# Kernel optimization log

Measured on AMD Instinct MI355X. Metric: run time of the kernel, lower is better.

## Reference

```python
import jax, jax.numpy as jnp
import numpy as np

N, E, B = 8000, 24000, 256
ATOM, BOND, H, HEADS, L = 133, 14, 256, 8, 5
NEG, EPS = 0.2, 1e-5


def _ln(x, g, b):
    m = x.mean(-1, keepdims=True)
    v = ((x - m) ** 2).mean(-1, keepdims=True)
    return (x - m) * jax.lax.rsqrt(v + EPS) * g + b


def setup_inputs() -> dict:
    key = jax.random.key(0)
    ks = jax.random.split(key, 12)
    s = lambda k, shp, fan: (jax.random.normal(k, shp, jnp.float32) / np.float32(np.sqrt(fan)))
    inp = {
        "x": jax.random.normal(ks[0], (N, ATOM), jnp.float32),
        "edge_attr": jax.random.normal(ks[1], (E, BOND), jnp.float32),
        "emb_W": s(ks[2], (ATOM, H), ATOM), "emb_b": jnp.zeros((H,), jnp.float32),
        "emb_g": jnp.ones((H,), jnp.float32), "emb_beta": jnp.zeros((H,), jnp.float32),
        "Wl": s(ks[3], (L, H, HEADS * H), H), "Wr": s(ks[4], (L, H, HEADS * H), H),
        "We": s(ks[5], (L, BOND, HEADS * H), BOND),
        "att": s(ks[6], (L, HEADS, H), H),
        "bias": jnp.zeros((L, H), jnp.float32),
        "ln_g": jnp.ones((L, H), jnp.float32), "ln_b": jnp.zeros((L, H), jnp.float32),
        "g1W": s(ks[7], (H, H // 2), H), "g1b": jnp.zeros((H // 2,), jnp.float32),
        "g2W": s(ks[8], (H // 2, 1), H // 2), "g2b": jnp.zeros((1,), jnp.float32),
        "edge_index": jax.random.randint(ks[9], (2, E), 0, N, dtype=jnp.int32),
        "batch_vec": jnp.sort(jax.random.randint(ks[10], (N,), 0, B, dtype=jnp.int32)),
    }
    return inp


def reference(x, edge_attr, emb_W, emb_b, emb_g, emb_beta, Wl, Wr, We, att, bias,
              ln_g, ln_b, g1W, g1b, g2W, g2b, edge_index, batch_vec):
    src, dst = edge_index[0], edge_index[1]
    # GATv2Conv add_self_loops=True, fill_value='mean': self-loop edge_attr at node i
    # is the mean of edge features of edges incoming to i (zeros if none).
    deg = jax.ops.segment_sum(jnp.ones((E,), x.dtype), dst, num_segments=N)
    loop_attr = jax.ops.segment_sum(edge_attr, dst, num_segments=N) / jnp.maximum(deg, 1.0)[:, None]
    ar = jnp.arange(N)
    src_a = jnp.concatenate([src, ar])
    dst_a = jnp.concatenate([dst, ar])
    ea = jnp.concatenate([edge_attr, loop_attr], axis=0)  # [E+N, BOND]
    # atom embedding: Linear -> LayerNorm -> ReLU (dropout = identity at eval)
    h = jax.nn.relu(_ln(x @ emb_W + emb_b, emb_g, emb_beta))  # [N, H]
    for l in range(L):
        xl = (h @ Wl[l]).reshape(N, HEADS, H)  # source transform
        xr = (h @ Wr[l]).reshape(N, HEADS, H)  # destination transform
        ee = (ea @ We[l]).reshape(-1, HEADS, H)
        f = jax.nn.leaky_relu(xl[src_a] + xr[dst_a] + ee, NEG)  # [EA, HEADS, H]
        score = jnp.einsum('ehd,hd->eh', f, att[l])  # [EA, HEADS]
        # scatter-softmax over edges sharing a destination (self-loops => no empty segment)
        m = jax.ops.segment_max(score, dst_a, num_segments=N)
        ex = jnp.exp(score - m[dst_a])
        alpha = ex / jax.ops.segment_sum(ex, dst_a, num_segments=N)[dst_a]
        msg = xl[src_a] * alpha[..., None]
        out = jax.ops.segment_sum(msg, dst_a, num_segments=N).mean(axis=1) + bias[l]  # concat=False: head mean
        h = _ln(out + h, ln_g[l], ln_b[l])  # residual + LayerNorm
    # GlobalAttention readout: gate_nn -> scatter-softmax per graph -> weighted sum
    gate = jax.nn.relu(h @ g1W + g1b) @ g2W + g2b  # [N, 1]
    gm = jax.ops.segment_max(gate, batch_vec, num_segments=B)
    ge = jnp.exp(gate - gm[batch_vec])
    w = ge / jnp.maximum(jax.ops.segment_sum(ge, batch_vec, num_segments=B)[batch_vec], 1e-16)
    return jax.ops.segment_sum(w * h, batch_vec, num_segments=B)  # [B, H]
```

## Files before the change

kernel.cpp:

```cpp
#include <hip/hip_runtime.h>
#include <math.h>

#define N_NODES 8000
#define N_EDGES 24000
#define NB      256
#define ATOM    133
#define BOND    14
#define HDIM    256
#define HEADS   8
#define NLAYERS 5
#define NEG     0.2f
#define LN_EPS  1e-5f
#define HH      (HEADS * HDIM)
#define MPAD    8064

typedef __attribute__((ext_vector_type(8))) short short8;
typedef __attribute__((ext_vector_type(4))) float floatx4;
typedef unsigned short ushort_t;

__device__ __forceinline__ ushort_t f2bf(float f) {
  unsigned u = __float_as_uint(f);
  unsigned r = (u + 0x7fff + ((u >> 16) & 1)) >> 16;
  return (ushort_t)r;
}
__device__ __forceinline__ float bf2f(ushort_t h) {
  return __uint_as_float(((unsigned)h) << 16);
}
__device__ __forceinline__ float4 ldbf4(const ushort_t* p) {
  ushort4 u = *(const ushort4*)p;
  return make_float4(bf2f(u.x), bf2f(u.y), bf2f(u.z), bf2f(u.w));
}

__device__ __forceinline__ void load_lds16(const void* g, void* l) {
  __builtin_amdgcn_global_load_lds((const __attribute__((address_space(1))) unsigned int*)g,
                                   (__attribute__((address_space(3))) unsigned int*)l,
                                   16, 0, 0);
}

__device__ __forceinline__ float block_reduce_sum(float v, float* red) {
  int t = threadIdx.x;
  red[t] = v; __syncthreads();
  for (int s = blockDim.x >> 1; s > 0; s >>= 1) {
    if (t < s) red[t] += red[t + s];
    __syncthreads();
  }
  float r = red[0]; __syncthreads();
  return r;
}
__device__ __forceinline__ float block_reduce_max(float v, float* red) {
  int t = threadIdx.x;
  red[t] = v; __syncthreads();
  for (int s = blockDim.x >> 1; s > 0; s >>= 1) {
    if (t < s) red[t] = fmaxf(red[t], red[t + s]);
    __syncthreads();
  }
  float r = red[0]; __syncthreads();
  return r;
}

__global__ void k_deg(const int* __restrict__ dst, int* __restrict__ deg) {
  int e = blockIdx.x * blockDim.x + threadIdx.x;
  if (e < N_EDGES) atomicAdd(&deg[dst[e]], 1);
}

__global__ void k_scan(const int* __restrict__ cnt, int* __restrict__ offs, int n) {
  __shared__ int wsum[8];
  __shared__ int carry_s;
  int t = threadIdx.x, w = t >> 6, lane = t & 63;
  if (t == 0) carry_s = 0;
  __syncthreads();
  for (int base = 0; base < n; base += 256) {
    int i = base + t;
    int v = (i < n) ? cnt[i] : 0;
    int x = v;
#pragma unroll
    for (int off = 1; off < 64; off <<= 1) {
      int u = __shfl_up(x, off);
      if (lane >= off) x += u;
    }
    if (lane == 63) wsum[w] = x;
    __syncthreads();
    int wpre = 0;
    for (int q = 0; q < w; q++) wpre += wsum[q];
    int carry = carry_s;
    if (i < n) offs[i] = carry + wpre + x - v;
    __syncthreads();
    if (t == 255) carry_s = carry + wpre + x;
    __syncthreads();
  }
  if (t == 0) offs[n] = carry_s;
}

__global__ void k_fill(const int* __restrict__ dst, const int* __restrict__ row_start,
                       int* __restrict__ cursor, int* __restrict__ csr_eid) {
  int e = blockIdx.x * blockDim.x + threadIdx.x;
  if (e < N_EDGES) {
    int d = dst[e];
    int pos = atomicAdd(&cursor[d], 1);
    csr_eid[row_start[d] + pos] = e;
  }
}

__global__ void k_loop_attr(const float* __restrict__ edge_attr, const int* __restrict__ row_start,
                            const int* __restrict__ csr_eid, float* __restrict__ loop_attr) {
  int t = blockIdx.x * blockDim.x + threadIdx.x;
  if (t >= N_NODES * BOND) return;
  int i = t / BOND, k = t % BOND;
  int beg = row_start[i], end = row_start[i + 1];
  float s = 0.f;
  for (int p = beg; p < end; p++) s += edge_attr[(size_t)csr_eid[p] * BOND + k];
  int degv = end - beg;
  loop_attr[(size_t)i * BOND + k] = s / fmaxf((float)degv, 1.f);
}

__global__ __launch_bounds__(256) void k_build_bt(const float* __restrict__ Wl,
                                                  const float* __restrict__ Wr,
                                                  ushort_t* __restrict__ Bt) {
  int l = blockIdx.x >> 12;
  int n = blockIdx.x & 4095;
  int k = threadIdx.x;
  const float* Wsrc = (n < HH) ? Wl : Wr;
  int nn = (n < HH) ? n : n - HH;
  float w = Wsrc[(size_t)l * HDIM * HH + (size_t)k * HH + nn];
  Bt[((size_t)l * 4096 + n) * 256 + k] = f2bf(w);
}

__global__ __launch_bounds__(256) void k_embed(const float* __restrict__ x, const float* __restrict__ W,
                                               const float* __restrict__ b, const float* __restrict__ g,
                                               const float* __restrict__ beta, float* __restrict__ h,
                                               ushort_t* __restrict__ Abuf) {
  __shared__ float xs[ATOM];
  __shared__ float red[256];
  int i = blockIdx.x, j = threadIdx.x;
  if (j < ATOM) xs[j] = x[(size_t)i * ATOM + j];
  __syncthreads();
  float acc = b[j];
  for (int k = 0; k < ATOM; k++) acc += xs[k] * W[(size_t)k * HDIM + j];
  float mean = block_reduce_sum(acc, red) * (1.f / HDIM);
  float diff = acc - mean;
  float var = block_reduce_sum(diff * diff, red) * (1.f / HDIM);
  float vn = diff * rsqrtf(var + LN_EPS) * g[j] + beta[j];
  float r = fmaxf(vn, 0.f);
  h[(size_t)i * HDIM + j] = r;
  Abuf[(size_t)i * 256 + j] = f2bf(r);
}

__global__ __launch_bounds__(256) void k_gemm_mfma(const ushort_t* __restrict__ A,
                                                   const ushort_t* __restrict__ Bt,
                                                   ushort_t* __restrict__ C) {
  __shared__ char smem[34816];
  ushort_t* As = (ushort_t*)smem;
  ushort_t* Bs = (ushort_t*)(smem + 16384);
  ushort_t* Cs = (ushort_t*)smem;
  const int tid = threadIdx.x;
  const int wave = tid >> 6, lane = tid & 63;
  const int bm = blockIdx.y * 128, bn = blockIdx.x * 128;
  const int wm = (wave >> 1) * 64, wn = (wave & 1) * 64;

  const ushort_t* agA[4];
  const ushort_t* agB[4];
  ushort_t* alA[4];
  ushort_t* alB[4];
#pragma unroll
  for (int j = 0; j < 4; j++) {
    int c = j * 256 + tid;
    int row = c >> 3, col = (c & 7) * 8;
    agA[j] = A  + (size_t)(bm + row) * 256 + col;
    agB[j] = Bt + (size_t)(bn + row) * 256 + col;
    alA[j] = As + c * 8;
    alB[j] = Bs + c * 8;
  }

  floatx4 acc[4][4] = {};
  const int mrow = lane & 15;
  const int kq = (lane >> 4) * 8;

  for (int k0 = 0; k0 < 256; k0 += 64) {
#pragma unroll
    for (int j = 0; j < 4; j++) load_lds16(agA[j] + k0, alA[j]);
#pragma unroll
    for (int j = 0; j < 4; j++) load_lds16(agB[j] + k0, alB[j]);
    __syncthreads();
#pragma unroll
    for (int half = 0; half < 2; half++) {
      const int kk = half * 32 + kq;
      short8 af[4], bfr[4];
#pragma unroll
      for (int mi = 0; mi < 4; mi++)
        af[mi] = *(const short8*)&As[(wm + mi * 16 + mrow) * 64 + kk];
#pragma unroll
      for (int ni = 0; ni < 4; ni++)
        bfr[ni] = *(const short8*)&Bs[(wn + ni * 16 + mrow) * 64 + kk];
#pragma unroll
      for (int mi = 0; mi < 4; mi++)
#pragma unroll
        for (int ni = 0; ni < 4; ni++)
          acc[mi][ni] = __builtin_amdgcn_mfma_f32_16x16x32_bf16(af[mi], bfr[ni], acc[mi][ni], 0, 0, 0);
    }
    __syncthreads();
  }
  const int lr = (lane >> 4) * 4, lc = lane & 15;
#pragma unroll
  for (int mi = 0; mi < 4; mi++)
#pragma unroll
    for (int ni = 0; ni < 4; ni++)
#pragma unroll
      for (int r = 0; r < 4; r++)
        Cs[(wm + mi * 16 + lr + r) * 136 + wn + ni * 16 + lc] = f2bf(acc[mi][ni][r]);
  __syncthreads();
#pragma unroll
  for (int it = 0; it < 8; it++) {
    int idx = it * 256 + tid;
    int row = idx >> 4, chunk = idx & 15;
    int grow = bm + row;
    if (grow < N_NODES) {
      short8 v = *(const short8*)&Cs[row * 136 + chunk * 8];
      *(short8*)&C[(size_t)grow * 4096 + bn + chunk * 8] = v;
    }
  }
}

__device__ __forceinline__ float edge_score(float x0, float x1, float x2, float x3,
                                            float r0, float r1, float r2, float r3,
                                            const float eav[BOND], const float wreg[BOND][4],
                                            float a0, float a1, float a2, float a3) {
  float e0 = 0.f, e1 = 0.f, e2 = 0.f, e3 = 0.f;
#pragma unroll
  for (int k = 0; k < BOND; k++) {
    e0 += eav[k] * wreg[k][0]; e1 += eav[k] * wreg[k][1];
    e2 += eav[k] * wreg[k][2]; e3 += eav[k] * wreg[k][3];
  }
  float f0 = x0 + r0 + e0; f0 = f0 > 0.f ? f0 : NEG * f0;
  float f1 = x1 + r1 + e1; f1 = f1 > 0.f ? f1 : NEG * f1;
  float f2 = x2 + r2 + e2; f2 = f2 > 0.f ? f2 : NEG * f2;
  float f3 = x3 + r3 + e3; f3 = f3 > 0.f ? f3 : NEG * f3;
  float sp = f0 * a0 + f1 * a1 + f2 * a2 + f3 * a3;
#pragma unroll
  for (int off = 32; off > 0; off >>= 1) sp += __shfl_xor(sp, off);
  return sp;
}

__device__ __forceinline__ void ld_eav(const float* p, float eav[BOND]) {
#pragma unroll
  for (int k = 0; k < 7; k++) {
    float2 t = *(const float2*)(p + 2 * k);
    eav[2 * k] = t.x; eav[2 * k + 1] = t.y;
  }
}

__global__ __launch_bounds__(512) void k_attn(const ushort_t* __restrict__ xlr,
    const float* __restrict__ edge_attr, const float* __restrict__ loop_attr,
    const float* __restrict__ We, const float* __restrict__ att,
    const int* __restrict__ row_start, const int* __restrict__ csr_eid,
    const int* __restrict__ src, const float* __restrict__ bias,
    const float* __restrict__ lng, const float* __restrict__ lnb,
    float* __restrict__ h, ushort_t* __restrict__ Abuf) {
  __shared__ ushort_t sacc[2][HEADS][264];
  const int tid = threadIdx.x, hh = tid >> 6, lane = tid & 63;
  float wreg[BOND][4];
#pragma unroll
  for (int k = 0; k < BOND; k++) {
    float4 t = *(const float4*)&We[(size_t)k * HH + hh * HDIM + lane * 4];
    wreg[k][0] = t.x; wreg[k][1] = t.y; wreg[k][2] = t.z; wreg[k][3] = t.w;
  }
  float4 at4 = *(const float4*)&att[hh * HDIM + lane * 4];
  const int node0 = blockIdx.x * 2;

#pragma unroll
  for (int ni = 0; ni < 2; ni++) {
    int i = node0 + ni;
    int beg = row_start[i], end = row_start[i + 1];
    float4 xr4 = ldbf4(&xlr[(size_t)i * 4096 + 2048 + hh * HDIM + lane * 4]);
    float4 xl4 = ldbf4(&xlr[(size_t)i * 4096 + hh * HDIM + lane * 4]);
    float eav[BOND];
    ld_eav(loop_attr + (size_t)i * BOND, eav);
    float4 px4;
    float peav[BOND];
    if (beg < end) {
      int e0 = csr_eid[beg];
      int sn0 = src[e0];
      px4 = ldbf4(&xlr[(size_t)sn0 * 4096 + hh * HDIM + lane * 4]);
      ld_eav(edge_attr + (size_t)e0 * BOND, peav);
    }
    float s = edge_score(xl4.x, xl4.y, xl4.z, xl4.w, xr4.x, xr4.y, xr4.z, xr4.w,
                         eav, wreg, at4.x, at4.y, at4.z, at4.w);
    float m = s, l = 1.f;
    float o0 = xl4.x, o1 = xl4.y, o2 = xl4.z, o3 = xl4.w;
    for (int p = beg; p < end; p++) {
      float4 x4 = px4;
      float ce[BOND];
#pragma unroll
      for (int k = 0; k < BOND; k++) ce[k] = peav[k];
      if (p + 1 < end) {
        int e2 = csr_eid[p + 1];
        int sn2 = src[e2];
        px4 = ldbf4(&xlr[(size_t)sn2 * 4096 + hh * HDIM + lane * 4]);
        ld_eav(edge_attr + (size_t)e2 * BOND, peav);
      }
      float s2 = edge_score(x4.x, x4.y, x4.z, x4.w, xr4.x, xr4.y, xr4.z, xr4.w,
                            ce, wreg, at4.x, at4.y, at4.z, at4.w);
      float mn = fmaxf(m, s2);
      float ca = __expf(m - mn), cb = __expf(s2 - mn);
      o0 = o0 * ca + x4.x * cb;
      o1 = o1 * ca + x4.y * cb;
      o2 = o2 * ca + x4.z * cb;
      o3 = o3 * ca + x4.w * cb;
      l = l * ca + cb;
      m = mn;
    }
    float inv = 1.f / l;
    ushort4 st;
    st.x = f2bf(o0 * inv); st.y = f2bf(o1 * inv);
    st.z = f2bf(o2 * inv); st.w = f2bf(o3 * inv);
    *(ushort4*)&sacc[ni][hh][lane * 4] = st;
  }
  __syncthreads();
  if (hh < 2) {
    int i = node0 + hh;
    float4 hres = *(const float4*)&h[(size_t)i * HDIM + lane * 4];
    float hr[4] = {hres.x, hres.y, hres.z, hres.w};
    float v[4] = {0.f, 0.f, 0.f, 0.f};
#pragma unroll
    for (int q = 0; q < HEADS; q++) {
      ushort4 u = *(const ushort4*)&sacc[hh][q][lane * 4];
      v[0] += bf2f(u.x); v[1] += bf2f(u.y); v[2] += bf2f(u.z); v[3] += bf2f(u.w);
    }
    float4 bias4 = *(const float4*)&bias[lane * 4];
    float bi[4] = {bias4.x, bias4.y, bias4.z, bias4.w};
#pragma unroll
    for (int j = 0; j < 4; j++) v[j] = v[j] * 0.125f + bi[j] + hr[j];
    float tot = v[0] + v[1] + v[2] + v[3];
#pragma unroll
    for (int off = 32; off > 0; off >>= 1) tot += __shfl_xor(tot, off);
    float mean = tot * (1.f / HDIM);
    float df[4], vr = 0.f;
#pragma unroll
    for (int j = 0; j < 4; j++) { df[j] = v[j] - mean; vr += df[j] * df[j]; }
#pragma unroll
    for (int off = 32; off > 0; off >>= 1) vr += __shfl_xor(vr, off);
    float rstd = rsqrtf(vr * (1.f / HDIM) + LN_EPS);
    float4 g4 = *(const float4*)&lng[lane * 4];
    float4 b4 = *(const float4*)&lnb[lane * 4];
    float gg[4] = {g4.x, g4.y, g4.z, g4.w};
    float bb[4] = {b4.x, b4.y, b4.z, b4.w};
    float r[4];
    ushort4 hi;
#pragma unroll
    for (int j = 0; j < 4; j++) r[j] = df[j] * rstd * gg[j] + bb[j];
    hi.x = f2bf(r[0]); hi.y = f2bf(r[1]); hi.z = f2bf(r[2]); hi.w = f2bf(r[3]);
    *(float4*)&h[(size_t)i * HDIM + lane * 4] = make_float4(r[0], r[1], r[2], r[3]);
    *(ushort4*)&Abuf[(size_t)i * 256 + lane * 4] = hi;
  }
}

__global__ __launch_bounds__(128) void k_gate(const float* __restrict__ h, const float* __restrict__ g1W,
                                              const float* __restrict__ g1b, const float* __restrict__ g2W,
                                              const float* __restrict__ g2b, float* __restrict__ gate) {
  __shared__ float hs[4][HDIM];
  __shared__ float red[4][132];
  const int j = threadIdx.x;
  const int i0 = blockIdx.x * 4;
#pragma unroll
  for (int it = 0; it < 2; it++) {
    int c = it * 128 + j;
    int node = c >> 6, off = (c & 63) * 4;
    *(float4*)&hs[node][off] = *(const float4*)&h[(size_t)(i0 + node) * HDIM + off];
  }
  __syncthreads();
  float acc[4];
  float b = g1b[j];
#pragma unroll
  for (int n = 0; n < 4; n++) acc[n] = b;
  for (int k = 0; k < HDIM; k++) {
    float w = g1W[(size_t)k * (HDIM / 2) + j];
#pragma unroll
    for (int n = 0; n < 4; n++) acc[n] += hs[n][k] * w;
  }
  float w2 = g2W[j];
#pragma unroll
  for (int n = 0; n < 4; n++) red[n][j] = fmaxf(acc[n], 0.f) * w2;
  __syncthreads();
  int n = j >> 5, l2 = j & 31;
  float s = red[n][l2] + red[n][l2 + 32] + red[n][l2 + 64] + red[n][l2 + 96];
#pragma unroll
  for (int off = 16; off > 0; off >>= 1) s += __shfl_xor(s, off, 32);
  if (l2 == 0) gate[i0 + n] = s + g2b[0];
}

__global__ void k_gcount(const int* __restrict__ batch, int* __restrict__ gcnt) {
  int i = blockIdx.x * blockDim.x + threadIdx.x;
  if (i < N_NODES) atomicAdd(&gcnt[batch[i]], 1);
}

__global__ __launch_bounds__(256) void k_readout(const float* __restrict__ h, const float* __restrict__ gate,
                                                 const int* __restrict__ goff, float* __restrict__ out) {
  __shared__ float red[256];
  int b = blockIdx.x, t = threadIdx.x;
  int beg = goff[b], end = goff[b + 1];
  if (end <= beg) { out[(size_t)b * HDIM + t] = 0.f; return; }
  float lm = -3.4e38f;
  for (int i = beg + t; i < end; i += 256) lm = fmaxf(lm, gate[i]);
  float m = block_reduce_max(lm, red);
  float ls = 0.f;
  for (int i = beg + t; i < end; i += 256) ls += __expf(gate[i] - m);
  float s = block_reduce_sum(ls, red);
  float inv = 1.f / fmaxf(s, 1e-16f);
  float acc = 0.f;
  for (int i = beg; i < end; i++) acc += __expf(gate[i] - m) * h[(size_t)i * HDIM + t];
  out[(size_t)b * HDIM + t] = acc * inv;
}

extern "C" void kernel_launch(void* const* d_in, const int* in_sizes, int n_in,
                              void* d_out, int out_size, void* d_ws, size_t ws_size,
                              hipStream_t stream) {
  const float* x         = (const float*)d_in[0];
  const float* edge_attr = (const float*)d_in[1];
  const float* emb_W     = (const float*)d_in[2];
  const float* emb_b     = (const float*)d_in[3];
  const float* emb_g     = (const float*)d_in[4];
  const float* emb_beta  = (const float*)d_in[5];
  const float* Wl        = (const float*)d_in[6];
  const float* Wr        = (const float*)d_in[7];
  const float* We        = (const float*)d_in[8];
  const float* att       = (const float*)d_in[9];
  const float* bias      = (const float*)d_in[10];
  const float* ln_g      = (const float*)d_in[11];
  const float* ln_b      = (const float*)d_in[12];
  const float* g1W       = (const float*)d_in[13];
  const float* g1b       = (const float*)d_in[14];
  const float* g2W       = (const float*)d_in[15];
  const float* g2b       = (const float*)d_in[16];
  const int*   edge_index= (const int*)d_in[17];
  const int*   batch     = (const int*)d_in[18];
  float* out = (float*)d_out;

  const int* src = edge_index;
  const int* dst = edge_index + N_EDGES;

  char* p = (char*)d_ws;
  auto alloc = [&](size_t bytes) -> void* {
    void* r = (void*)p;
    p += (bytes + 255) & ~(size_t)255;
    return r;
  };
  int*   deg       = (int*)alloc((size_t)N_NODES * 4);
  int*   row_start = (int*)alloc((size_t)(N_NODES + 1) * 4);
  int*   cursor    = (int*)alloc((size_t)N_NODES * 4);
  int*   csr_eid   = (int*)alloc((size_t)N_EDGES * 4);
  float* loop_attr = (float*)alloc((size_t)N_NODES * BOND * 4);
  float* h         = (float*)alloc((size_t)N_NODES * HDIM * 4);
  ushort_t* Abuf   = (ushort_t*)alloc((size_t)MPAD * 256 * 2);
  ushort_t* Bt     = (ushort_t*)alloc((size_t)NLAYERS * 4096 * 256 * 2);
  ushort_t* xlr    = (ushort_t*)alloc((size_t)N_NODES * 4096 * 2);
  float* gate      = (float*)alloc((size_t)N_NODES * 4);
  int*   gcnt      = (int*)alloc((size_t)NB * 4);
  int*   goff      = (int*)alloc((size_t)(NB + 1) * 4);

  hipMemsetAsync(deg, 0, (size_t)N_NODES * 4, stream);
  hipMemsetAsync(cursor, 0, (size_t)N_NODES * 4, stream);
  hipMemsetAsync(gcnt, 0, (size_t)NB * 4, stream);

  k_deg<<<(N_EDGES + 255) / 256, 256, 0, stream>>>(dst, deg);
  k_scan<<<1, 256, 0, stream>>>(deg, row_start, N_NODES);
  k_fill<<<(N_EDGES + 255) / 256, 256, 0, stream>>>(dst, row_start, cursor, csr_eid);
  k_loop_attr<<<(N_NODES * BOND + 255) / 256, 256, 0, stream>>>(edge_attr, row_start, csr_eid, loop_attr);
  k_build_bt<<<NLAYERS * 4096, 256, 0, stream>>>(Wl, Wr, Bt);
  k_embed<<<N_NODES, 256, 0, stream>>>(x, emb_W, emb_b, emb_g, emb_beta, h, Abuf);

  dim3 ggrid(4096 / 128, MPAD / 128);
  for (int l = 0; l < NLAYERS; l++) {
    const ushort_t* Bt_l = Bt + (size_t)l * 4096 * 256;
    const float* We_l  = We + (size_t)l * BOND * HH;
    const float* att_l = att + (size_t)l * HEADS * HDIM;
    k_gemm_mfma<<<ggrid, 256, 0, stream>>>(Abuf, Bt_l, xlr);
    k_attn<<<4000, 512, 0, stream>>>(xlr, edge_attr, loop_attr, We_l, att_l,
                                     row_start, csr_eid, src,
                                     bias + (size_t)l * HDIM, ln_g + (size_t)l * HDIM,
                                     ln_b + (size_t)l * HDIM, h, Abuf);
  }

  k_gate<<<N_NODES / 4, 128, 0, stream>>>(h, g1W, g1b, g2W, g2b, gate);
  k_gcount<<<(N_NODES + 255) / 256, 256, 0, stream>>>(batch, gcnt);
  k_scan<<<1, 256, 0, stream>>>(gcnt, goff, NB);
  k_readout<<<NB, 256, 0, stream>>>(h, gate, goff, out);
}
```

Before: 849.5 us.

## Split attention into edge-parallel score kernel and node aggregation kernel

The fused per-node attention kernel is split in two. A new edge-parallel kernel computes all edge scores per head into a transposed score buffer, with each wave handling 64 CSR-ordered edges and prefetching the next one. A separate aggregation kernel then does a two-pass softmax (max, then exp-sum) and gathers source features. This spreads the score work evenly across edges instead of across nodes with uneven degree, at the cost of an extra launch, re-reading xl rows and a score round-trip through memory. The weight-transpose kernel is also rewritten to stage tiles in LDS and emit vector stores.

New measurement: 929.2 us. +9.4%, slower.

```diff
diff --git a/kernel.cpp b/kernel.cpp
--- a/kernel.cpp
+++ b/kernel.cpp
@@ -13,6 +13,7 @@
 #define LN_EPS  1e-5f
 #define HH      (HEADS * HDIM)
 #define MPAD    8064
+#define EA      (N_EDGES + N_NODES)
 
 typedef __attribute__((ext_vector_type(8))) short short8;
 typedef __attribute__((ext_vector_type(4))) float floatx4;
@@ -91,13 +92,18 @@
   if (t == 0) offs[n] = carry_s;
 }
 
-__global__ void k_fill(const int* __restrict__ dst, const int* __restrict__ row_start,
-                       int* __restrict__ cursor, int* __restrict__ csr_eid) {
+__global__ void k_fill(const int* __restrict__ src, const int* __restrict__ dst,
+                       const int* __restrict__ row_start, int* __restrict__ cursor,
+                       int* __restrict__ csr_eid, int* __restrict__ csr_src,
+                       int* __restrict__ csr_dst) {
   int e = blockIdx.x * blockDim.x + threadIdx.x;
   if (e < N_EDGES) {
     int d = dst[e];
     int pos = atomicAdd(&cursor[d], 1);
-    csr_eid[row_start[d] + pos] = e;
+    int q = row_start[d] + pos;
+    csr_eid[q] = e;
+    csr_src[q] = src[e];
+    csr_dst[q] = d;
   }
 }
 
@@ -116,13 +122,30 @@
 __global__ __launch_bounds__(256) void k_build_bt(const float* __restrict__ Wl,
                                                   const float* __restrict__ Wr,
                                                   ushort_t* __restrict__ Bt) {
-  int l = blockIdx.x >> 12;
-  int n = blockIdx.x & 4095;
-  int k = threadIdx.x;
+  __shared__ ushort_t s[64 * 40];
+  int l = blockIdx.x >> 6;
+  int n0 = (blockIdx.x & 63) * 64;
+  int t = threadIdx.x;
+  int nl = t & 63;
+  int kr = t >> 6;
+  int n = n0 + nl;
   const float* Wsrc = (n < HH) ? Wl : Wr;
   int nn = (n < HH) ? n : n - HH;
-  float w = Wsrc[(size_t)l * HDIM * HH + (size_t)k * HH + nn];
-  Bt[((size_t)l * 4096 + n) * 256 + k] = f2bf(w);
+  const float* base = Wsrc + (size_t)l * HDIM * HH + nn;
+  for (int kb = 0; kb < 256; kb += 32) {
+#pragma unroll
+    for (int q = 0; q < 8; q++) {
+      int k = kb + q * 4 + kr;
+      s[nl * 40 + q * 4 + kr] = f2bf(base[(size_t)k * HH]);
+    }
+    __syncthreads();
+    {
+      int n2 = t >> 2, c = t & 3;
+      short8 v = *(const short8*)&s[n2 * 40 + c * 8];
+      *(short8*)&Bt[((size_t)l * 4096 + n0 + n2) * 256 + kb + c * 8] = v;
+    }
+    __syncthreads();
+  }
 }
 
 __global__ __launch_bounds__(256) void k_embed(const float* __restrict__ x, const float* __restrict__ W,
@@ -248,67 +271,100 @@
   }
 }
 
-__global__ __launch_bounds__(512) void k_attn(const ushort_t* __restrict__ xlr,
+__global__ __launch_bounds__(256) void k_score(const ushort_t* __restrict__ xlr,
     const float* __restrict__ edge_attr, const float* __restrict__ loop_attr,
     const float* __restrict__ We, const float* __restrict__ att,
-    const int* __restrict__ row_start, const int* __restrict__ csr_eid,
-    const int* __restrict__ src, const float* __restrict__ bias,
+    const int* __restrict__ csr_src, const int* __restrict__ csr_dst,
+    const int* __restrict__ csr_eid, float* __restrict__ score_T) {
+  const int tid = threadIdx.x, w = tid >> 6, lane = tid & 63;
+  const int hh = blockIdx.y;
+  float wreg[BOND][4];
+#pragma unroll
+  for (int k = 0; k < BOND; k++) {
+    float4 t = *(const float4*)&We[(size_t)k * HH + hh * HDIM + lane * 4];
+    wreg[k][0] = t.x; wreg[k][1] = t.y; wreg[k][2] = t.z; wreg[k][3] = t.w;
+  }
+  float4 at4 = *(const float4*)&att[hh * HDIM + lane * 4];
+
+  const int p0 = (blockIdx.x * 4 + w) * 64;
+  const bool tail = (p0 >= N_EDGES);
+  int sj, dj, ej;
+  if (!tail) {
+    sj = csr_src[p0 + lane];
+    dj = csr_dst[p0 + lane];
+    ej = csr_eid[p0 + lane];
+  } else {
+    sj = dj = ej = p0 + lane - N_EDGES;
+  }
+  const float* featb = tail ? loop_attr : edge_attr;
+
+  int s_n = __builtin_amdgcn_readlane(sj, 0);
+  int d_n = __builtin_amdgcn_readlane(dj, 0);
+  int e_n = __builtin_amdgcn_readlane(ej, 0);
+  float4 xl4 = ldbf4(&xlr[(size_t)s_n * 4096 + hh * HDIM + lane * 4]);
+  float4 xr4 = ldbf4(&xlr[(size_t)d_n * 4096 + 2048 + hh * HDIM + lane * 4]);
+  float eav[BOND];
+  ld_eav(featb + (size_t)e_n * BOND, eav);
+
+  float sacc = 0.f;
+  for (int j = 0; j < 64; j++) {
+    float4 cxl = xl4, cxr = xr4;
+    float ce[BOND];
+#pragma unroll
+    for (int k = 0; k < BOND; k++) ce[k] = eav[k];
+    if (j < 63) {
+      s_n = __builtin_amdgcn_readlane(sj, j + 1);
+      d_n = __builtin_amdgcn_readlane(dj, j + 1);
+      e_n = __builtin_amdgcn_readlane(ej, j + 1);
+      xl4 = ldbf4(&xlr[(size_t)s_n * 4096 + hh * HDIM + lane * 4]);
+      xr4 = ldbf4(&xlr[(size_t)d_n * 4096 + 2048 + hh * HDIM + lane * 4]);
+      ld_eav(featb + (size_t)e_n * BOND, eav);
+    }
+    float sp = edge_score(cxl.x, cxl.y, cxl.z, cxl.w, cxr.x, cxr.y, cxr.z, cxr.w,
+                          ce, wreg, at4.x, at4.y, at4.z, at4.w);
+    sacc = (lane == j) ? sp : sacc;
+  }
+  score_T[(size_t)hh * EA + p0 + lane] = sacc;
+}
+
+__global__ __launch_bounds__(512) void k_agg(const ushort_t* __restrict__ xlr,
+    const float* __restrict__ score_T, const int* __restrict__ row_start,
+    const int* __restrict__ csr_src, const float* __restrict__ bias,
     const float* __restrict__ lng, const float* __restrict__ lnb,
     float* __restrict__ h, ushort_t* __restrict__ Abuf) {
   __shared__ ushort_t sacc[2][HEADS][264];
   const int tid = threadIdx.x, hh = tid >> 6, lane = tid & 63;
-  float wreg[BOND][4];
-#pragma unroll
-  for (int k = 0; k < BOND; k++) {
-    float4 t = *(const float4*)&We[(size_t)k * HH + hh * HDIM + lane * 4];
-    wreg[k][0] = t.x; wreg[k][1] = t.y; wreg[k][2] = t.z; wreg[k][3] = t.w;
-  }
-  float4 at4 = *(const float4*)&att[hh * HDIM + lane * 4];
   const int node0 = blockIdx.x * 2;
+  const float* sc = score_T + (size_t)hh * EA;
 
 #pragma unroll
   for (int ni = 0; ni < 2; ni++) {
     int i = node0 + ni;
     int beg = row_start[i], end = row_start[i + 1];
-    float4 xr4 = ldbf4(&xlr[(size_t)i * 4096 + 2048 + hh * HDIM + lane * 4]);
-    float4 xl4 = ldbf4(&xlr[(size_t)i * 4096 + hh * HDIM + lane * 4]);
-    float eav[BOND];
-    ld_eav(loop_attr + (size_t)i * BOND, eav);
-    float4 px4;
-    float peav[BOND];
+    float s_self = sc[N_EDGES + i];
+    float m = s_self;
+    for (int p = beg; p < end; p++) m = fmaxf(m, sc[p]);
+    float4 px;
+    int pn;
     if (beg < end) {
-      int e0 = csr_eid[beg];
-      int sn0 = src[e0];
-      px4 = ldbf4(&xlr[(size_t)sn0 * 4096 + hh * HDIM + lane * 4]);
-      ld_eav(edge_attr + (size_t)e0 * BOND, peav);
-    }
-    float s = edge_score(xl4.x, xl4.y, xl4.z, xl4.w, xr4.x, xr4.y, xr4.z, xr4.w,
-                         eav, wreg, at4.x, at4.y, at4.z, at4.w);
-    float m = s, l = 1.f;
-    float o0 = xl4.x, o1 = xl4.y, o2 = xl4.z, o3 = xl4.w;
+      pn = csr_src[beg];
+      px = ldbf4(&xlr[(size_t)pn * 4096 + hh * HDIM + lane * 4]);
+    }
+    float w0 = __expf(s_self - m);
+    float denom = w0;
+    float4 xi = ldbf4(&xlr[(size_t)i * 4096 + hh * HDIM + lane * 4]);
+    float o0 = w0 * xi.x, o1 = w0 * xi.y, o2 = w0 * xi.z, o3 = w0 * xi.w;
     for (int p = beg; p < end; p++) {
-      float4 x4 = px4;
-      float ce[BOND];
-#pragma unroll
-      for (int k = 0; k < BOND; k++) ce[k] = peav[k];
+      float4 x4 = px;
       if (p + 1 < end) {
-        int e2 = csr_eid[p + 1];
-        int sn2 = src[e2];
-        px4 = ldbf4(&xlr[(size_t)sn2 * 4096 + hh * HDIM + lane * 4]);
-        ld_eav(edge_attr + (size_t)e2 * BOND, peav);
+        pn = csr_src[p + 1];
+        px = ldbf4(&xlr[(size_t)pn * 4096 + hh * HDIM + lane * 4]);
       }
-      float s2 = edge_score(x4.x, x4.y, x4.z, x4.w, xr4.x, xr4.y, xr4.z, xr4.w,
-                            ce, wreg, at4.x, at4.y, at4.z, at4.w);
-      float mn = fmaxf(m, s2);
-      float ca = __expf(m - mn), cb = __expf(s2 - mn);
-      o0 = o0 * ca + x4.x * cb;
-      o1 = o1 * ca + x4.y * cb;
-      o2 = o2 * ca + x4.z * cb;
-      o3 = o3 * ca + x4.w * cb;
-      l = l * ca + cb;
-      m = mn;
-    }
-    float inv = 1.f / l;
+      float wv = __expf(sc[p] - m);
+      denom += wv;
+      o0 += wv * x4.x; o1 += wv * x4.y; o2 += wv * x4.z; o3 += wv * x4.w;
+    }
+    float inv = 1.f / denom;
     ushort4 st;
     st.x = f2bf(o0 * inv); st.y = f2bf(o1 * inv);
     st.z = f2bf(o2 * inv); st.w = f2bf(o3 * inv);
@@ -447,11 +503,14 @@
   int*   row_start = (int*)alloc((size_t)(N_NODES + 1) * 4);
   int*   cursor    = (int*)alloc((size_t)N_NODES * 4);
   int*   csr_eid   = (int*)alloc((size_t)N_EDGES * 4);
+  int*   csr_src   = (int*)alloc((size_t)N_EDGES * 4);
+  int*   csr_dst   = (int*)alloc((size_t)N_EDGES * 4);
   float* loop_attr = (float*)alloc((size_t)N_NODES * BOND * 4);
   float* h         = (float*)alloc((size_t)N_NODES * HDIM * 4);
   ushort_t* Abuf   = (ushort_t*)alloc((size_t)MPAD * 256 * 2);
   ushort_t* Bt     = (ushort_t*)alloc((size_t)NLAYERS * 4096 * 256 * 2);
   ushort_t* xlr    = (ushort_t*)alloc((size_t)N_NODES * 4096 * 2);
+  float* score_T   = (float*)alloc((size_t)HEADS * EA * 4);
   float* gate      = (float*)alloc((size_t)N_NODES * 4);
   int*   gcnt      = (int*)alloc((size_t)NB * 4);
   int*   goff      = (int*)alloc((size_t)(NB + 1) * 4);
@@ -462,9 +521,10 @@
 
   k_deg<<<(N_EDGES + 255) / 256, 256, 0, stream>>>(dst, deg);
   k_scan<<<1, 256, 0, stream>>>(deg, row_start, N_NODES);
-  k_fill<<<(N_EDGES + 255) / 256, 256, 0, stream>>>(dst, row_start, cursor, csr_eid);
+  k_fill<<<(N_EDGES + 255) / 256, 256, 0, stream>>>(src, dst, row_start, cursor,
+                                                    csr_eid, csr_src, csr_dst);
   k_loop_attr<<<(N_NODES * BOND + 255) / 256, 256, 0, stream>>>(edge_attr, row_start, csr_eid, loop_attr);
-  k_build_bt<<<NLAYERS * 4096, 256, 0, stream>>>(Wl, Wr, Bt);
+  k_build_bt<<<NLAYERS * 64, 256, 0, stream>>>(Wl, Wr, Bt);
   k_embed<<<N_NODES, 256, 0, stream>>>(x, emb_W, emb_b, emb_g, emb_beta, h, Abuf);
 
   dim3 ggrid(4096 / 128, MPAD / 128);
@@ -473,10 +533,11 @@
     const float* We_l  = We + (size_t)l * BOND * HH;
     const float* att_l = att + (size_t)l * HEADS * HDIM;
     k_gemm_mfma<<<ggrid, 256, 0, stream>>>(Abuf, Bt_l, xlr);
-    k_attn<<<4000, 512, 0, stream>>>(xlr, edge_attr, loop_attr, We_l, att_l,
-                                     row_start, csr_eid, src,
-                                     bias + (size_t)l * HDIM, ln_g + (size_t)l * HDIM,
-                                     ln_b + (size_t)l * HDIM, h, Abuf);
+    k_score<<<dim3(EA / 256, HEADS), 256, 0, stream>>>(xlr, edge_attr, loop_attr, We_l, att_l,
+                                                       csr_src, csr_dst, csr_eid, score_T);
+    k_agg<<<N_NODES / 2, 512, 0, stream>>>(xlr, score_T, row_start, csr_src,
+                                           bias + (size_t)l * HDIM, ln_g + (size_t)l * HDIM,
+                                           ln_b + (size_t)l * HDIM, h, Abuf);
   }
 
   k_gate<<<N_NODES / 4, 128, 0, stream>>>(h, g1W, g1b, g2W, g2b, gate);
```
